# Kernel optimization log

Hardware: AMD Instinct MI355X
Metric: run time of the kernel (lower is better)

Reference implementation:

```python
import jax, jax.numpy as jnp
import numpy as np

N_GENES = 20000   # num_all_genes
D = 256           # embedding_dim
NNZ = 640000      # nonzeros in GO adjacency (~32 avg degree)
N_COND = 2000     # number of conditions
B = 16384         # batch size
MAXG = 5          # max_genes_per_condition
L = 2             # num_gnn_layers


def setup_inputs() -> dict:
    key = jax.random.key(0)
    ks = jax.random.split(key, 12)
    cond_idx = jax.random.randint(ks[0], (B,), 0, N_COND, dtype=jnp.int32)
    pert_embedding = jax.random.normal(ks[1], (N_GENES, D), jnp.float32) * 0.05
    gnn_kernels = jax.random.normal(ks[2], (L, D, D), jnp.float32) * 0.05
    mlp_w1 = jax.random.normal(ks[3], (D, D), jnp.float32) * 0.05
    mlp_b1 = jnp.zeros((D,), jnp.float32)
    mlp_w2 = jax.random.normal(ks[4], (D, D), jnp.float32) * 0.05
    mlp_b2 = jnp.zeros((D,), jnp.float32)
    adj_row = jax.random.randint(ks[5], (NNZ,), 0, N_GENES, dtype=jnp.int64)
    adj_col = jax.random.randint(ks[6], (NNZ,), 0, N_GENES, dtype=jnp.int64)
    adj_vals = jax.random.uniform(ks[7], (NNZ,), jnp.float32)
    cond_gene_idx = jax.random.randint(ks[8], (N_COND, MAXG), 0, N_GENES, dtype=jnp.int32)
    counts = jax.random.randint(ks[9], (N_COND,), 0, MAXG + 1)
    cond_gene_mask = (jnp.arange(MAXG)[None, :] < counts[:, None]).astype(jnp.float32)
    # padded slots get -1 index like the original (later clamped to 0)
    cond_gene_idx = jnp.where(cond_gene_mask > 0, cond_gene_idx, -1)
    return {
        'cond_idx': cond_idx,
        'pert_embedding': pert_embedding,
        'gnn_kernels': gnn_kernels,
        'mlp_w1': mlp_w1, 'mlp_b1': mlp_b1,
        'mlp_w2': mlp_w2, 'mlp_b2': mlp_b2,
        'adj_row': adj_row, 'adj_col': adj_col, 'adj_vals': adj_vals,
        'cond_gene_idx': cond_gene_idx, 'cond_gene_mask': cond_gene_mask,
    }


def reference(cond_idx, pert_embedding, gnn_kernels, mlp_w1, mlp_b1,
              mlp_w2, mlp_b2, adj_row, adj_col, adj_vals,
              cond_gene_idx, cond_gene_mask):
    # --- GNN over the full gene graph (sparse adjacency @ dense emb, then dense kernel) ---
    emb = pert_embedding  # [N, D]
    for i in range(L):
        # SpMM: aggregated[r] = sum_{nnz with row r} vals * emb[col]
        msgs = adj_vals[:, None] * emb[adj_col]            # [NNZ, D]
        agg = jax.ops.segment_sum(msgs, adj_row, num_segments=N_GENES)  # [N, D]
        emb = agg @ gnn_kernels[i]                          # [N, D]
        if i < L - 1:
            emb = jax.nn.relu(emb)

    # --- per-condition gather of up to MAXG gene embeddings, masked sum ---
    gidx = cond_gene_idx[cond_idx]          # [B, MAXG] int
    gmask = cond_gene_mask[cond_idx]        # [B, MAXG]
    gidx_safe = jnp.maximum(gidx, 0)
    gene_embs = emb[gidx_safe]              # [B, MAXG, D]
    summed = jnp.sum(gene_embs * gmask[:, :, None], axis=1)  # [B, D]
    n_genes = jnp.sum(gmask, axis=1)        # [B]

    # --- small MLP (applied when n_genes > 1), identity when ==1, zeros when ==0 ---
    h = jax.nn.relu(summed @ mlp_w1 + mlp_b1)
    mlp_out = jax.nn.relu(h @ mlp_w2 + mlp_b2)  # [B, D]

    n = n_genes[:, None]
    out = jnp.where(n == 0.0, 0.0, jnp.where(n == 1.0, summed, mlp_out))
    return out
```

## Files before the change

### kernel.cpp

```cpp
#include <hip/hip_runtime.h>

static constexpr int N_GENES = 20000;
static constexpr int D       = 256;
static constexpr int NNZ     = 640000;
static constexpr int BATCH   = 16384;
static constexpr int MAXG    = 5;
static constexpr int SCAN_B  = (N_GENES + 255) / 256;

using bf16x8 = __attribute__((ext_vector_type(8))) short;
using f32x4  = __attribute__((ext_vector_type(4))) float;

__device__ __forceinline__ unsigned short f2bf(float f) {
  unsigned int u = __builtin_bit_cast(unsigned int, f);
  u += 0x7fffu + ((u >> 16) & 1u);
  return (unsigned short)(u >> 16);
}
__device__ __forceinline__ float bf2f(unsigned short h) {
  unsigned int u = ((unsigned int)h) << 16;
  return __builtin_bit_cast(float, u);
}
__device__ __forceinline__ void gload16(const void* g, void* l) {
  __builtin_amdgcn_global_load_lds(
      (const __attribute__((address_space(1))) unsigned int*)g,
      (__attribute__((address_space(3))) unsigned int*)l, 16, 0, 0);
}

__global__ void zero_int(int* __restrict__ p, int n) {
  int i = blockIdx.x * blockDim.x + threadIdx.x;
  if (i < n) p[i] = 0;
}

__global__ void count_rows(const int* __restrict__ adj_row, int* __restrict__ cnt) {
  int e = blockIdx.x * blockDim.x + threadIdx.x;
  if (e < NNZ) atomicAdd(&cnt[adj_row[e]], 1);
}

__global__ __launch_bounds__(256)
void scan_partial(const int* __restrict__ cnt, int* __restrict__ bsum) {
  __shared__ int red[256];
  int b = blockIdx.x, t = threadIdx.x, i = b * 256 + t;
  red[t] = (i < N_GENES) ? cnt[i] : 0;
  __syncthreads();
  for (int off = 128; off > 0; off >>= 1) {
    if (t < off) red[t] += red[t + off];
    __syncthreads();
  }
  if (t == 0) bsum[b] = red[0];
}

__global__ __launch_bounds__(256)
void scan_final2(const int* __restrict__ cnt, const int* __restrict__ bsum,
                 int* __restrict__ row_ptr, int* __restrict__ fill_ctr) {
  __shared__ int bs[128];
  __shared__ int s[256];
  int b = blockIdx.x, t = threadIdx.x, i = b * 256 + t;
  if (t < 128) bs[t] = (t < SCAN_B) ? bsum[t] : 0;
  __syncthreads();
  for (int off = 1; off < 128; off <<= 1) {
    int v = (t >= off && t < 128) ? bs[t - off] : 0;
    __syncthreads();
    if (t < 128) bs[t] += v;
    __syncthreads();
  }
  int bpre = (b == 0) ? 0 : bs[b - 1];
  int x = (i < N_GENES) ? cnt[i] : 0;
  s[t] = x;
  __syncthreads();
  for (int off = 1; off < 256; off <<= 1) {
    int v = (t >= off) ? s[t - off] : 0;
    __syncthreads();
    s[t] += v;
    __syncthreads();
  }
  if (i < N_GENES) {
    int e = bpre + s[t] - x;
    row_ptr[i] = e;
    fill_ctr[i] = e;
  }
  if (b == 0 && t == 0) row_ptr[N_GENES] = NNZ;
}

__global__ __launch_bounds__(256)
void fused_fill_conv(const int* __restrict__ adj_row, const int* __restrict__ adj_col,
                     const float* __restrict__ vals, int* __restrict__ fill_ctr,
                     unsigned int* __restrict__ edges,
                     const float* __restrict__ gk, const float* __restrict__ w1,
                     const float* __restrict__ w2,
                     char* __restrict__ whi, char* __restrict__ wlo,
                     const float* __restrict__ pert, ushort4* __restrict__ pert_bf) {
  int b = blockIdx.x, t = threadIdx.x;
  if (b < 2500) {
    int e = b * 256 + t;
    int r = adj_row[e];
    int p = atomicAdd(&fill_ctr[r], 1);
    edges[p] = (unsigned int)adj_col[e] | ((unsigned int)f2bf(vals[e]) << 16);
  } else if (b < 2628) {
    int g = (b - 2500) * 256 + t;
    int wid = g >> 13, rest = g & 8191;
    const float* W = (wid == 0) ? gk : (wid == 1) ? gk + 65536 : (wid == 2) ? w1 : w2;
    int c  = rest >> 9;
    int nc = c >> 2, kt = c & 3;
    int o  = (rest & 511) << 4;
    int n  = o >> 7;
    int wb = (o & 127) ^ ((n & 7) << 4);
    int k  = wb >> 1;
    size_t obase = ((size_t)wid << 17) + ((size_t)c << 13) + o;
    unsigned short* ph = (unsigned short*)(whi + obase);
    unsigned short* pl = (unsigned short*)(wlo + obase);
    #pragma unroll
    for (int e2 = 0; e2 < 8; ++e2) {
      float f = W[(size_t)(kt * 64 + k + e2) * 256 + nc * 64 + n];
      unsigned short h = f2bf(f);
      ph[e2] = h;
      pl[e2] = f2bf(f - bf2f(h));
    }
  } else {
    int i = (b - 2628) * 256 + t;
    float4 v = reinterpret_cast<const float4*>(pert)[i];
    ushort4 r4;
    r4.x = f2bf(v.x); r4.y = f2bf(v.y); r4.z = f2bf(v.z); r4.w = f2bf(v.w);
    pert_bf[i] = r4;
  }
}

__global__ __launch_bounds__(256)
void spmm_csr_img(const int* __restrict__ row_ptr, const unsigned int* __restrict__ edges,
                  const unsigned short* __restrict__ src,
                  char* __restrict__ hi_img, char* __restrict__ lo_img) {
  int row = blockIdx.x * 4 + (threadIdx.x >> 6);
  int lane = threadIdx.x & 63;
  int beg = row_ptr[row], end = row_ptr[row + 1];
  const unsigned short* sp = src + lane * 4;
  float4 acc = {0.f, 0.f, 0.f, 0.f};
  int j = beg;
  for (; j + 8 <= end; j += 8) {
    unsigned int e0 = edges[j],     e1 = edges[j + 1], e2 = edges[j + 2], e3 = edges[j + 3];
    unsigned int e4 = edges[j + 4], e5 = edges[j + 5], e6 = edges[j + 6], e7 = edges[j + 7];
    ushort4 g0 = *reinterpret_cast<const ushort4*>(sp + (size_t)(e0 & 0xFFFFu) * D);
    ushort4 g1 = *reinterpret_cast<const ushort4*>(sp + (size_t)(e1 & 0xFFFFu) * D);
    ushort4 g2 = *reinterpret_cast<const ushort4*>(sp + (size_t)(e2 & 0xFFFFu) * D);
    ushort4 g3 = *reinterpret_cast<const ushort4*>(sp + (size_t)(e3 & 0xFFFFu) * D);
    ushort4 g4 = *reinterpret_cast<const ushort4*>(sp + (size_t)(e4 & 0xFFFFu) * D);
    ushort4 g5 = *reinterpret_cast<const ushort4*>(sp + (size_t)(e5 & 0xFFFFu) * D);
    ushort4 g6 = *reinterpret_cast<const ushort4*>(sp + (size_t)(e6 & 0xFFFFu) * D);
    ushort4 g7 = *reinterpret_cast<const ushort4*>(sp + (size_t)(e7 & 0xFFFFu) * D);
    float v0 = bf2f(e0 >> 16), v1 = bf2f(e1 >> 16), v2 = bf2f(e2 >> 16), v3 = bf2f(e3 >> 16);
    float v4 = bf2f(e4 >> 16), v5 = bf2f(e5 >> 16), v6 = bf2f(e6 >> 16), v7 = bf2f(e7 >> 16);
    acc.x += v0 * bf2f(g0.x); acc.y += v0 * bf2f(g0.y); acc.z += v0 * bf2f(g0.z); acc.w += v0 * bf2f(g0.w);
    acc.x += v1 * bf2f(g1.x); acc.y += v1 * bf2f(g1.y); acc.z += v1 * bf2f(g1.z); acc.w += v1 * bf2f(g1.w);
    acc.x += v2 * bf2f(g2.x); acc.y += v2 * bf2f(g2.y); acc.z += v2 * bf2f(g2.z); acc.w += v2 * bf2f(g2.w);
    acc.x += v3 * bf2f(g3.x); acc.y += v3 * bf2f(g3.y); acc.z += v3 * bf2f(g3.z); acc.w += v3 * bf2f(g3.w);
    acc.x += v4 * bf2f(g4.x); acc.y += v4 * bf2f(g4.y); acc.z += v4 * bf2f(g4.z); acc.w += v4 * bf2f(g4.w);
    acc.x += v5 * bf2f(g5.x); acc.y += v5 * bf2f(g5.y); acc.z += v5 * bf2f(g5.z); acc.w += v5 * bf2f(g5.w);
    acc.x += v6 * bf2f(g6.x); acc.y += v6 * bf2f(g6.y); acc.z += v6 * bf2f(g6.z); acc.w += v6 * bf2f(g6.w);
    acc.x += v7 * bf2f(g7.x); acc.y += v7 * bf2f(g7.y); acc.z += v7 * bf2f(g7.z); acc.w += v7 * bf2f(g7.w);
  }
  for (; j < end; ++j) {
    unsigned int e = edges[j];
    ushort4 g = *reinterpret_cast<const ushort4*>(sp + (size_t)(e & 0xFFFFu) * D);
    float v = bf2f(e >> 16);
    acc.x += v * bf2f(g.x); acc.y += v * bf2f(g.y); acc.z += v * bf2f(g.z); acc.w += v * bf2f(g.w);
  }
  int mt = row >> 7, r = row & 127, kt = lane >> 4;
  int wb = ((lane & 15) << 3) ^ ((r & 7) << 4);
  size_t off = ((size_t)(mt * 4 + kt) << 14) + (size_t)r * 128 + wb;
  float a4[4] = {acc.x, acc.y, acc.z, acc.w};
  ushort4 hi, lo;
  unsigned short* ph = (unsigned short*)&hi;
  unsigned short* pl = (unsigned short*)&lo;
  #pragma unroll
  for (int e = 0; e < 4; ++e) {
    unsigned short h = f2bf(a4[e]);
    ph[e] = h;
    pl[e] = f2bf(a4[e] - bf2f(h));
  }
  *reinterpret_cast<ushort4*>(hi_img + off) = hi;
  *reinterpret_cast<ushort4*>(lo_img + off) = lo;
}

__global__ __launch_bounds__(256)
void gather_conditions(const int* __restrict__ cond_idx, const int* __restrict__ cg_idx,
                       const float* __restrict__ cg_mask, const float* __restrict__ emb,
                       float* __restrict__ out, char* __restrict__ hi_img,
                       char* __restrict__ lo_img, float* __restrict__ ngenes) {
  int b = blockIdx.x * 4 + (threadIdx.x >> 6);
  int lane = threadIdx.x & 63;
  int c = cond_idx[b];
  float4 acc = {0.f, 0.f, 0.f, 0.f};
  float n = 0.f;
  #pragma unroll
  for (int g = 0; g < MAXG; ++g) {
    float m = cg_mask[c * MAXG + g];
    n += m;
    if (m > 0.f) {
      int gi = cg_idx[c * MAXG + g];
      float4 e = *reinterpret_cast<const float4*>(emb + (size_t)gi * D + lane * 4);
      acc.x += m * e.x; acc.y += m * e.y; acc.z += m * e.z; acc.w += m * e.w;
    }
  }
  *reinterpret_cast<float4*>(out + (size_t)b * D + lane * 4) = acc;
  int mt = b >> 7, r = b & 127, kt = lane >> 4;
  int wb = ((lane & 15) << 3) ^ ((r & 7) << 4);
  size_t off = ((size_t)(mt * 4 + kt) << 14) + (size_t)r * 128 + wb;
  float a4[4] = {acc.x, acc.y, acc.z, acc.w};
  ushort4 hi, lo;
  unsigned short* ph = (unsigned short*)&hi;
  unsigned short* pl = (unsigned short*)&lo;
  #pragma unroll
  for (int e = 0; e < 4; ++e) {
    unsigned short h = f2bf(a4[e]);
    ph[e] = h;
    pl[e] = f2bf(a4[e] - bf2f(h));
  }
  *reinterpret_cast<ushort4*>(hi_img + off) = hi;
  *reinterpret_cast<ushort4*>(lo_img + off) = lo;
  if (lane == 0) ngenes[b] = n;
}

enum Epi { E_F32, E_RELU_BF16, E_HIMG, E_SELECT };

template <Epi EP>
__global__ __launch_bounds__(256)
void gemm_bf16x3(const char* __restrict__ Ahi, const char* __restrict__ Alo,
                 const char* __restrict__ Bhi, const char* __restrict__ Blo,
                 const float* __restrict__ bias, float* __restrict__ C,
                 unsigned short* __restrict__ Cbf,
                 char* __restrict__ Ohi, char* __restrict__ Olo,
                 const float* __restrict__ ngenes, int M) {
  __shared__ __align__(16) char smem[65536];
  char* sAh = smem;
  char* sAl = smem + 16384;
  char* sBh = smem + 32768;
  char* sBl = smem + 49152;

  const int t = threadIdx.x;
  const int w = t >> 6, l = t & 63;
  const int wr = w >> 1, wc = w & 1;

  const int nwg  = gridDim.x;
  const int orig = blockIdx.x;
  const int xcd = orig & 7, boff = orig >> 3;
  const int q = nwg >> 3, r8 = nwg & 7;
  const int wgid = (xcd < r8 ? xcd * (q + 1) : r8 * (q + 1) + (xcd - r8) * q) + boff;
  const int mt = wgid >> 1, nt2 = wgid & 1;

  f32x4 acc[4][4] = {};

  const int rA = l & 15;
  const int kB = (l >> 4) << 4;
  const int xA = (rA & 7) << 4;

  for (int kt = 0; kt < 4; ++kt) {
    const char* gAh  = Ahi + ((size_t)(mt * 4 + kt) << 14);
    const char* gAl  = Alo + ((size_t)(mt * 4 + kt) << 14);
    const char* gBh0 = Bhi + ((size_t)((nt2 * 2 + 0) * 4 + kt) << 13);
    const char* gBl0 = Blo + ((size_t)((nt2 * 2 + 0) * 4 + kt) << 13);
    const char* gBh1 = Bhi + ((size_t)((nt2 * 2 + 1) * 4 + kt) << 13);
    const char* gBl1 = Blo + ((size_t)((nt2 * 2 + 1) * 4 + kt) << 13);
    #pragma unroll
    for (int j = 0; j < 4; ++j) {
      gload16(gAh + (j * 256 + t) * 16, sAh + j * 4096 + w * 1024);
      gload16(gAl + (j * 256 + t) * 16, sAl + j * 4096 + w * 1024);
    }
    #pragma unroll
    for (int j = 0; j < 2; ++j) {
      gload16(gBh0 + (j * 256 + t) * 16, sBh + j * 4096 + w * 1024);
      gload16(gBl0 + (j * 256 + t) * 16, sBl + j * 4096 + w * 1024);
    }
    #pragma unroll
    for (int j = 0; j < 2; ++j) {
      gload16(gBh1 + (j * 256 + t) * 16, sBh + 8192 + j * 4096 + w * 1024);
      gload16(gBl1 + (j * 256 + t) * 16, sBl + 8192 + j * 4096 + w * 1024);
    }
    asm volatile("s_waitcnt vmcnt(0)" ::: "memory");
    __syncthreads();
    #pragma unroll
    for (int ks = 0; ks < 2; ++ks) {
      bf16x8 ah[4], al[4], bh[4], bl[4];
      #pragma unroll
      for (int i = 0; i < 4; ++i) {
        int r   = wr * 64 + i * 16 + rA;
        int off = r * 128 + ((ks * 64 + kB) ^ xA);
        ah[i] = *(const bf16x8*)(sAh + off);
        al[i] = *(const bf16x8*)(sAl + off);
      }
      #pragma unroll
      for (int j = 0; j < 4; ++j) {
        int n   = wc * 64 + j * 16 + rA;
        int off = n * 128 + ((ks * 64 + kB) ^ xA);
        bh[j] = *(const bf16x8*)(sBh + off);
        bl[j] = *(const bf16x8*)(sBl + off);
      }
      #pragma unroll
      for (int i = 0; i < 4; ++i)
        #pragma unroll
        for (int j = 0; j < 4; ++j) {
          acc[i][j] = __builtin_amdgcn_mfma_f32_16x16x32_bf16(ah[i], bh[j], acc[i][j], 0, 0, 0);
          acc[i][j] = __builtin_amdgcn_mfma_f32_16x16x32_bf16(ah[i], bl[j], acc[i][j], 0, 0, 0);
          acc[i][j] = __builtin_amdgcn_mfma_f32_16x16x32_bf16(al[i], bh[j], acc[i][j], 0, 0, 0);
        }
    }
    __syncthreads();
  }

  const int cr = (l >> 4) << 2;
  const int cc = l & 15;
  #pragma unroll
  for (int i = 0; i < 4; ++i) {
    #pragma unroll
    for (int rr = 0; rr < 4; ++rr) {
      int rin  = wr * 64 + i * 16 + cr + rr;
      int grow = mt * 128 + rin;
      if (grow >= M) continue;
      bool wr_row = true;
      if (EP == E_SELECT) wr_row = (ngenes[grow] >= 1.5f);
      #pragma unroll
      for (int j = 0; j < 4; ++j) {
        float v    = acc[i][j][rr];
        int colin  = wc * 64 + j * 16 + cc;
        int gcol   = nt2 * 128 + colin;
        if (EP == E_HIMG || EP == E_SELECT) v += bias[gcol];
        if (EP != E_F32) v = fmaxf(v, 0.f);
        if (EP == E_HIMG) {
          int kt2 = nt2 * 2 + (colin >> 6);
          int k2  = colin & 63;
          int wb  = (k2 << 1) ^ ((rin & 7) << 4);
          size_t off = ((size_t)(mt * 4 + kt2) << 14) + (size_t)rin * 128 + wb;
          unsigned short h16 = f2bf(v);
          *(unsigned short*)(Ohi + off) = h16;
          *(unsigned short*)(Olo + off) = f2bf(v - bf2f(h16));
        } else if (EP == E_RELU_BF16) {
          Cbf[(size_t)grow * 256 + gcol] = f2bf(v);
        } else if (wr_row) {
          C[(size_t)grow * 256 + gcol] = v;
        }
      }
    }
  }
}

extern "C" void kernel_launch(void* const* d_in, const int* in_sizes, int n_in,
                              void* d_out, int out_size, void* d_ws, size_t ws_size,
                              hipStream_t stream) {
  const int*   cond_idx = (const int*)d_in[0];
  const float* pert     = (const float*)d_in[1];
  const float* gnn_k    = (const float*)d_in[2];
  const float* w1       = (const float*)d_in[3];
  const float* b1       = (const float*)d_in[4];
  const float* w2       = (const float*)d_in[5];
  const float* b2       = (const float*)d_in[6];
  const int*   adj_row  = (const int*)d_in[7];
  const int*   adj_col  = (const int*)d_in[8];
  const float* adj_vals = (const float*)d_in[9];
  const int*   cg_idx   = (const int*)d_in[10];
  const float* cg_mask  = (const float*)d_in[11];
  float* out = (float*)d_out;

  char* w = (char*)d_ws;
  auto alloc = [&](size_t bytes) {
    void* p = w;
    w += (bytes + 255) & ~size_t(255);
    return p;
  };
  constexpr int MT_G = (N_GENES + 127) / 128;
  constexpr int MT_B = BATCH / 128;
  char*         aggHi   = (char*)alloc((size_t)MT_G * 4 * 16384);
  char*         aggLo   = (char*)alloc((size_t)MT_G * 4 * 16384);
  float*        embf    = (float*)alloc((size_t)N_GENES * D * 4);
  char*         sumHi   = (char*)alloc((size_t)MT_B * 4 * 16384);
  char*         sumLo   = (char*)alloc((size_t)MT_B * 4 * 16384);
  char*         hHi     = (char*)alloc((size_t)MT_B * 4 * 16384);
  char*         hLo     = (char*)alloc((size_t)MT_B * 4 * 16384);
  char*         wHi     = (char*)alloc((size_t)4 << 17);
  char*         wLo     = (char*)alloc((size_t)4 << 17);
  unsigned int* edges   = (unsigned int*)alloc((size_t)NNZ * 4);
  int*          cnt     = (int*)alloc((size_t)N_GENES * 4);
  int*          row_ptr = (int*)alloc((size_t)(N_GENES + 4) * 4);
  int*          fill_ctr= (int*)alloc((size_t)N_GENES * 4);
  int*          bsum    = (int*)alloc((size_t)128 * 4);
  float*        ngenes  = (float*)alloc((size_t)BATCH * 4);

  unsigned short* pert_bf = (unsigned short*)hHi;
  unsigned short* embf_bf = (unsigned short*)embf;

  zero_int<<<(N_GENES + 255) / 256, 256, 0, stream>>>(cnt, N_GENES);
  count_rows<<<NNZ / 256, 256, 0, stream>>>(adj_row, cnt);
  scan_partial<<<SCAN_B, 256, 0, stream>>>(cnt, bsum);
  scan_final2<<<SCAN_B, 256, 0, stream>>>(cnt, bsum, row_ptr, fill_ctr);
  fused_fill_conv<<<2500 + 128 + 5000, 256, 0, stream>>>(
      adj_row, adj_col, adj_vals, fill_ctr, edges,
      gnn_k, w1, w2, wHi, wLo, pert, (ushort4*)pert_bf);

  spmm_csr_img<<<N_GENES / 4, 256, 0, stream>>>(row_ptr, edges, pert_bf, aggHi, aggLo);
  gemm_bf16x3<E_RELU_BF16><<<2 * MT_G, 256, 0, stream>>>(
      aggHi, aggLo, wHi, wLo, nullptr, nullptr, embf_bf, nullptr, nullptr, nullptr, N_GENES);

  spmm_csr_img<<<N_GENES / 4, 256, 0, stream>>>(row_ptr, edges, embf_bf, aggHi, aggLo);
  gemm_bf16x3<E_F32><<<2 * MT_G, 256, 0, stream>>>(
      aggHi, aggLo, wHi + (1 << 17), wLo + (1 << 17), nullptr, embf, nullptr, nullptr, nullptr, nullptr, N_GENES);

  gather_conditions<<<BATCH / 4, 256, 0, stream>>>(cond_idx, cg_idx, cg_mask, embf,
                                                   out, sumHi, sumLo, ngenes);

  gemm_bf16x3<E_HIMG><<<2 * MT_B, 256, 0, stream>>>(
      sumHi, sumLo, wHi + (2 << 17), wLo + (2 << 17), b1, nullptr, nullptr, hHi, hLo, nullptr, BATCH);

  gemm_bf16x3<E_SELECT><<<2 * MT_B, 256, 0, stream>>>(
      hHi, hLo, wHi + (3 << 17), wLo + (3 << 17), b2, out, nullptr, nullptr, nullptr, ngenes, BATCH);
}
```

Before: 314.6 us.

## Fuse condition gather into first MLP GEMM and merge scan kernels

Moves the per-condition masked gather of gene embeddings into the first MLP GEMM. Each block builds its bf16 hi/lo A tile directly in shared memory, which removes the separate gather kernel and its sum-image round trip through global memory. The two-pass prefix scan becomes a single kernel in which each block recomputes its own prefix from the counts. Zeroing the counts now uses hipMemsetAsync. The cost is that both column-half blocks redo the same gather, and that gather now runs serially before the MFMA work in each k-step.

After: 326.2 us. 3.7% more time.

```diff
diff --git a/kernel.cpp b/kernel.cpp
--- a/kernel.cpp
+++ b/kernel.cpp
@@ -8,6 +8,7 @@
 static constexpr int SCAN_B  = (N_GENES + 255) / 256;
 
 using bf16x8 = __attribute__((ext_vector_type(8))) short;
+using us8    = __attribute__((ext_vector_type(8))) unsigned short;
 using f32x4  = __attribute__((ext_vector_type(4))) float;
 
 __device__ __forceinline__ unsigned short f2bf(float f) {
@@ -25,44 +26,26 @@
       (__attribute__((address_space(3))) unsigned int*)l, 16, 0, 0);
 }
 
-__global__ void zero_int(int* __restrict__ p, int n) {
-  int i = blockIdx.x * blockDim.x + threadIdx.x;
-  if (i < n) p[i] = 0;
-}
-
 __global__ void count_rows(const int* __restrict__ adj_row, int* __restrict__ cnt) {
   int e = blockIdx.x * blockDim.x + threadIdx.x;
   if (e < NNZ) atomicAdd(&cnt[adj_row[e]], 1);
 }
 
 __global__ __launch_bounds__(256)
-void scan_partial(const int* __restrict__ cnt, int* __restrict__ bsum) {
-  __shared__ int red[256];
+void scan_one(const int* __restrict__ cnt, int* __restrict__ row_ptr,
+              int* __restrict__ fill_ctr) {
+  __shared__ int s[256];
   int b = blockIdx.x, t = threadIdx.x, i = b * 256 + t;
-  red[t] = (i < N_GENES) ? cnt[i] : 0;
+  int pre_t = 0;
+  for (int c = 0; c < b; ++c) pre_t += cnt[c * 256 + t];
+  s[t] = pre_t;
   __syncthreads();
   for (int off = 128; off > 0; off >>= 1) {
-    if (t < off) red[t] += red[t + off];
-    __syncthreads();
-  }
-  if (t == 0) bsum[b] = red[0];
-}
-
-__global__ __launch_bounds__(256)
-void scan_final2(const int* __restrict__ cnt, const int* __restrict__ bsum,
-                 int* __restrict__ row_ptr, int* __restrict__ fill_ctr) {
-  __shared__ int bs[128];
-  __shared__ int s[256];
-  int b = blockIdx.x, t = threadIdx.x, i = b * 256 + t;
-  if (t < 128) bs[t] = (t < SCAN_B) ? bsum[t] : 0;
+    if (t < off) s[t] += s[t + off];
+    __syncthreads();
+  }
+  int bpre = s[0];
   __syncthreads();
-  for (int off = 1; off < 128; off <<= 1) {
-    int v = (t >= off && t < 128) ? bs[t - off] : 0;
-    __syncthreads();
-    if (t < 128) bs[t] += v;
-    __syncthreads();
-  }
-  int bpre = (b == 0) ? 0 : bs[b - 1];
   int x = (i < N_GENES) ? cnt[i] : 0;
   s[t] = x;
   __syncthreads();
@@ -178,46 +161,13 @@
   *reinterpret_cast<ushort4*>(lo_img + off) = lo;
 }
 
-__global__ __launch_bounds__(256)
-void gather_conditions(const int* __restrict__ cond_idx, const int* __restrict__ cg_idx,
-                       const float* __restrict__ cg_mask, const float* __restrict__ emb,
-                       float* __restrict__ out, char* __restrict__ hi_img,
-                       char* __restrict__ lo_img, float* __restrict__ ngenes) {
-  int b = blockIdx.x * 4 + (threadIdx.x >> 6);
-  int lane = threadIdx.x & 63;
-  int c = cond_idx[b];
-  float4 acc = {0.f, 0.f, 0.f, 0.f};
-  float n = 0.f;
-  #pragma unroll
-  for (int g = 0; g < MAXG; ++g) {
-    float m = cg_mask[c * MAXG + g];
-    n += m;
-    if (m > 0.f) {
-      int gi = cg_idx[c * MAXG + g];
-      float4 e = *reinterpret_cast<const float4*>(emb + (size_t)gi * D + lane * 4);
-      acc.x += m * e.x; acc.y += m * e.y; acc.z += m * e.z; acc.w += m * e.w;
-    }
-  }
-  *reinterpret_cast<float4*>(out + (size_t)b * D + lane * 4) = acc;
-  int mt = b >> 7, r = b & 127, kt = lane >> 4;
-  int wb = ((lane & 15) << 3) ^ ((r & 7) << 4);
-  size_t off = ((size_t)(mt * 4 + kt) << 14) + (size_t)r * 128 + wb;
-  float a4[4] = {acc.x, acc.y, acc.z, acc.w};
-  ushort4 hi, lo;
-  unsigned short* ph = (unsigned short*)&hi;
-  unsigned short* pl = (unsigned short*)&lo;
-  #pragma unroll
-  for (int e = 0; e < 4; ++e) {
-    unsigned short h = f2bf(a4[e]);
-    ph[e] = h;
-    pl[e] = f2bf(a4[e] - bf2f(h));
-  }
-  *reinterpret_cast<ushort4*>(hi_img + off) = hi;
-  *reinterpret_cast<ushort4*>(lo_img + off) = lo;
-  if (lane == 0) ngenes[b] = n;
-}
-
-enum Epi { E_F32, E_RELU_BF16, E_HIMG, E_SELECT };
+__device__ __forceinline__ int xcd_swizzle(int orig, int nwg) {
+  int xcd = orig & 7, boff = orig >> 3;
+  int q = nwg >> 3, r8 = nwg & 7;
+  return (xcd < r8 ? xcd * (q + 1) : r8 * (q + 1) + (xcd - r8) * q) + boff;
+}
+
+enum Epi { E_F32, E_RELU_BF16, E_SELECT };
 
 template <Epi EP>
 __global__ __launch_bounds__(256)
@@ -225,7 +175,6 @@
                  const char* __restrict__ Bhi, const char* __restrict__ Blo,
                  const float* __restrict__ bias, float* __restrict__ C,
                  unsigned short* __restrict__ Cbf,
-                 char* __restrict__ Ohi, char* __restrict__ Olo,
                  const float* __restrict__ ngenes, int M) {
   __shared__ __align__(16) char smem[65536];
   char* sAh = smem;
@@ -236,16 +185,10 @@
   const int t = threadIdx.x;
   const int w = t >> 6, l = t & 63;
   const int wr = w >> 1, wc = w & 1;
-
-  const int nwg  = gridDim.x;
-  const int orig = blockIdx.x;
-  const int xcd = orig & 7, boff = orig >> 3;
-  const int q = nwg >> 3, r8 = nwg & 7;
-  const int wgid = (xcd < r8 ? xcd * (q + 1) : r8 * (q + 1) + (xcd - r8) * q) + boff;
+  const int wgid = xcd_swizzle(blockIdx.x, gridDim.x);
   const int mt = wgid >> 1, nt2 = wgid & 1;
 
   f32x4 acc[4][4] = {};
-
   const int rA = l & 15;
   const int kB = (l >> 4) << 4;
   const int xA = (rA & 7) << 4;
@@ -266,9 +209,6 @@
     for (int j = 0; j < 2; ++j) {
       gload16(gBh0 + (j * 256 + t) * 16, sBh + j * 4096 + w * 1024);
       gload16(gBl0 + (j * 256 + t) * 16, sBl + j * 4096 + w * 1024);
-    }
-    #pragma unroll
-    for (int j = 0; j < 2; ++j) {
       gload16(gBh1 + (j * 256 + t) * 16, sBh + 8192 + j * 4096 + w * 1024);
       gload16(gBl1 + (j * 256 + t) * 16, sBl + 8192 + j * 4096 + w * 1024);
     }
@@ -279,15 +219,13 @@
       bf16x8 ah[4], al[4], bh[4], bl[4];
       #pragma unroll
       for (int i = 0; i < 4; ++i) {
-        int r   = wr * 64 + i * 16 + rA;
-        int off = r * 128 + ((ks * 64 + kB) ^ xA);
+        int off = (wr * 64 + i * 16 + rA) * 128 + ((ks * 64 + kB) ^ xA);
         ah[i] = *(const bf16x8*)(sAh + off);
         al[i] = *(const bf16x8*)(sAl + off);
       }
       #pragma unroll
       for (int j = 0; j < 4; ++j) {
-        int n   = wc * 64 + j * 16 + rA;
-        int off = n * 128 + ((ks * 64 + kB) ^ xA);
+        int off = (wc * 64 + j * 16 + rA) * 128 + ((ks * 64 + kB) ^ xA);
         bh[j] = *(const bf16x8*)(sBh + off);
         bl[j] = *(const bf16x8*)(sBl + off);
       }
@@ -316,24 +254,148 @@
       if (EP == E_SELECT) wr_row = (ngenes[grow] >= 1.5f);
       #pragma unroll
       for (int j = 0; j < 4; ++j) {
-        float v    = acc[i][j][rr];
-        int colin  = wc * 64 + j * 16 + cc;
-        int gcol   = nt2 * 128 + colin;
-        if (EP == E_HIMG || EP == E_SELECT) v += bias[gcol];
+        float v   = acc[i][j][rr];
+        int gcol  = nt2 * 128 + wc * 64 + j * 16 + cc;
+        if (EP == E_SELECT) v += bias[gcol];
         if (EP != E_F32) v = fmaxf(v, 0.f);
-        if (EP == E_HIMG) {
-          int kt2 = nt2 * 2 + (colin >> 6);
-          int k2  = colin & 63;
-          int wb  = (k2 << 1) ^ ((rin & 7) << 4);
-          size_t off = ((size_t)(mt * 4 + kt2) << 14) + (size_t)rin * 128 + wb;
-          unsigned short h16 = f2bf(v);
-          *(unsigned short*)(Ohi + off) = h16;
-          *(unsigned short*)(Olo + off) = f2bf(v - bf2f(h16));
-        } else if (EP == E_RELU_BF16) {
+        if (EP == E_RELU_BF16) {
           Cbf[(size_t)grow * 256 + gcol] = f2bf(v);
         } else if (wr_row) {
           C[(size_t)grow * 256 + gcol] = v;
         }
+      }
+    }
+  }
+}
+
+__global__ __launch_bounds__(256)
+void gemm_mlp1(const int* __restrict__ cond_idx, const int* __restrict__ cg_idx,
+               const float* __restrict__ cg_mask, const float* __restrict__ embf,
+               const char* __restrict__ Bhi, const char* __restrict__ Blo,
+               const float* __restrict__ bias, float* __restrict__ out,
+               float* __restrict__ ngenes,
+               char* __restrict__ Ohi, char* __restrict__ Olo) {
+  __shared__ __align__(16) char smem[65536];
+  char* sAh = smem;
+  char* sAl = smem + 16384;
+  char* sBh = smem + 32768;
+  char* sBl = smem + 49152;
+
+  const int t = threadIdx.x;
+  const int w = t >> 6, l = t & 63;
+  const int wr = w >> 1, wc = w & 1;
+  const int wgid = xcd_swizzle(blockIdx.x, gridDim.x);
+  const int mt = wgid >> 1, nt2 = wgid & 1;
+
+  const int gr = t >> 1, ghalf = t & 1;
+  const int grow = mt * 128 + gr;
+  const int gc = cond_idx[grow];
+
+  f32x4 acc[4][4] = {};
+  const int rA = l & 15;
+  const int kB = (l >> 4) << 4;
+  const int xA = (rA & 7) << 4;
+
+  for (int kt = 0; kt < 4; ++kt) {
+    const char* gBh0 = Bhi + ((size_t)((nt2 * 2 + 0) * 4 + kt) << 13);
+    const char* gBl0 = Blo + ((size_t)((nt2 * 2 + 0) * 4 + kt) << 13);
+    const char* gBh1 = Bhi + ((size_t)((nt2 * 2 + 1) * 4 + kt) << 13);
+    const char* gBl1 = Blo + ((size_t)((nt2 * 2 + 1) * 4 + kt) << 13);
+    #pragma unroll
+    for (int j = 0; j < 2; ++j) {
+      gload16(gBh0 + (j * 256 + t) * 16, sBh + j * 4096 + w * 1024);
+      gload16(gBl0 + (j * 256 + t) * 16, sBl + j * 4096 + w * 1024);
+      gload16(gBh1 + (j * 256 + t) * 16, sBh + 8192 + j * 4096 + w * 1024);
+      gload16(gBl1 + (j * 256 + t) * 16, sBl + 8192 + j * 4096 + w * 1024);
+    }
+    float4 a[8] = {};
+    float n = 0.f;
+    #pragma unroll
+    for (int g = 0; g < MAXG; ++g) {
+      float m = cg_mask[gc * MAXG + g];
+      n += m;
+      if (m > 0.f) {
+        const float4* e = reinterpret_cast<const float4*>(
+            embf + (size_t)cg_idx[gc * MAXG + g] * 256 + kt * 64 + ghalf * 32);
+        #pragma unroll
+        for (int q = 0; q < 8; ++q) {
+          float4 ev = e[q];
+          a[q].x += m * ev.x; a[q].y += m * ev.y;
+          a[q].z += m * ev.z; a[q].w += m * ev.w;
+        }
+      }
+    }
+    if (nt2 == 0) {
+      float4* o = reinterpret_cast<float4*>(out + (size_t)grow * 256 + kt * 64 + ghalf * 32);
+      #pragma unroll
+      for (int q = 0; q < 8; ++q) o[q] = a[q];
+      if (kt == 0 && ghalf == 0) ngenes[grow] = n;
+    }
+    const int xr = (gr & 7) << 4;
+    const float* av = reinterpret_cast<const float*>(a);
+    #pragma unroll
+    for (int q = 0; q < 4; ++q) {
+      us8 hv, lv;
+      #pragma unroll
+      for (int jj = 0; jj < 8; ++jj) {
+        float vv = av[q * 8 + jj];
+        unsigned short h = f2bf(vv);
+        hv[jj] = h;
+        lv[jj] = f2bf(vv - bf2f(h));
+      }
+      int byteoff = gr * 128 + (((ghalf * 32 + q * 8) << 1) ^ xr);
+      *reinterpret_cast<us8*>(sAh + byteoff) = hv;
+      *reinterpret_cast<us8*>(sAl + byteoff) = lv;
+    }
+    asm volatile("s_waitcnt vmcnt(0)" ::: "memory");
+    __syncthreads();
+    #pragma unroll
+    for (int ks = 0; ks < 2; ++ks) {
+      bf16x8 ah[4], al[4], bh[4], bl[4];
+      #pragma unroll
+      for (int i = 0; i < 4; ++i) {
+        int off = (wr * 64 + i * 16 + rA) * 128 + ((ks * 64 + kB) ^ xA);
+        ah[i] = *(const bf16x8*)(sAh + off);
+        al[i] = *(const bf16x8*)(sAl + off);
+      }
+      #pragma unroll
+      for (int j = 0; j < 4; ++j) {
+        int off = (wc * 64 + j * 16 + rA) * 128 + ((ks * 64 + kB) ^ xA);
+        bh[j] = *(const bf16x8*)(sBh + off);
+        bl[j] = *(const bf16x8*)(sBl + off);
+      }
+      #pragma unroll
+      for (int i = 0; i < 4; ++i)
+        #pragma unroll
+        for (int j = 0; j < 4; ++j) {
+          acc[i][j] = __builtin_amdgcn_mfma_f32_16x16x32_bf16(ah[i], bh[j], acc[i][j], 0, 0, 0);
+          acc[i][j] = __builtin_amdgcn_mfma_f32_16x16x32_bf16(ah[i], bl[j], acc[i][j], 0, 0, 0);
+          acc[i][j] = __builtin_amdgcn_mfma_f32_16x16x32_bf16(al[i], bh[j], acc[i][j], 0, 0, 0);
+        }
+    }
+    __syncthreads();
+  }
+
+  const int cr = (l >> 4) << 2;
+  const int cc = l & 15;
+  #pragma unroll
+  for (int i = 0; i < 4; ++i) {
+    #pragma unroll
+    for (int rr = 0; rr < 4; ++rr) {
+      int rin = wr * 64 + i * 16 + cr + rr;
+      #pragma unroll
+      for (int j = 0; j < 4; ++j) {
+        float v   = acc[i][j][rr];
+        int colin = wc * 64 + j * 16 + cc;
+        int gcol  = nt2 * 128 + colin;
+        v = fmaxf(v + bias[gcol], 0.f);
+        int kt2 = nt2 * 2 + (colin >> 6);
+        int k2  = colin & 63;
+        int wb  = (k2 << 1) ^ ((rin & 7) << 4);
+        size_t off = ((size_t)(mt * 4 + kt2) << 14) + (size_t)rin * 128 + wb;
+        unsigned short h16 = f2bf(v);
+        *(unsigned short*)(Ohi + off) = h16;
+        *(unsigned short*)(Olo + off) = f2bf(v - bf2f(h16));
       }
     }
   }
@@ -367,8 +429,6 @@
   char*         aggHi   = (char*)alloc((size_t)MT_G * 4 * 16384);
   char*         aggLo   = (char*)alloc((size_t)MT_G * 4 * 16384);
   float*        embf    = (float*)alloc((size_t)N_GENES * D * 4);
-  char*         sumHi   = (char*)alloc((size_t)MT_B * 4 * 16384);
-  char*         sumLo   = (char*)alloc((size_t)MT_B * 4 * 16384);
   char*         hHi     = (char*)alloc((size_t)MT_B * 4 * 16384);
   char*         hLo     = (char*)alloc((size_t)MT_B * 4 * 16384);
   char*         wHi     = (char*)alloc((size_t)4 << 17);
@@ -377,34 +437,31 @@
   int*          cnt     = (int*)alloc((size_t)N_GENES * 4);
   int*          row_ptr = (int*)alloc((size_t)(N_GENES + 4) * 4);
   int*          fill_ctr= (int*)alloc((size_t)N_GENES * 4);
-  int*          bsum    = (int*)alloc((size_t)128 * 4);
   float*        ngenes  = (float*)alloc((size_t)BATCH * 4);
-
-  unsigned short* pert_bf = (unsigned short*)hHi;
+  char*         pertbf_buf = (char*)alloc((size_t)N_GENES * D * 2);
+
+  unsigned short* pert_bf = (unsigned short*)pertbf_buf;
   unsigned short* embf_bf = (unsigned short*)embf;
 
-  zero_int<<<(N_GENES + 255) / 256, 256, 0, stream>>>(cnt, N_GENES);
+  hipMemsetAsync(cnt, 0, (size_t)N_GENES * 4, stream);
   count_rows<<<NNZ / 256, 256, 0, stream>>>(adj_row, cnt);
-  scan_partial<<<SCAN_B, 256, 0, stream>>>(cnt, bsum);
-  scan_final2<<<SCAN_B, 256, 0, stream>>>(cnt, bsum, row_ptr, fill_ctr);
+  scan_one<<<SCAN_B, 256, 0, stream>>>(cnt, row_ptr, fill_ctr);
   fused_fill_conv<<<2500 + 128 + 5000, 256, 0, stream>>>(
       adj_row, adj_col, adj_vals, fill_ctr, edges,
       gnn_k, w1, w2, wHi, wLo, pert, (ushort4*)pert_bf);
 
   spmm_csr_img<<<N_GENES / 4, 256, 0, stream>>>(row_ptr, edges, pert_bf, aggHi, aggLo);
   gemm_bf16x3<E_RELU_BF16><<<2 * MT_G, 256, 0, stream>>>(
-      aggHi, aggLo, wHi, wLo, nullptr, nullptr, embf_bf, nullptr, nullptr, nullptr, N_GENES);
+      aggHi, aggLo, wHi, wLo, nullptr, nullptr, embf_bf, nullptr, N_GENES);
 
   spmm_csr_img<<<N_GENES / 4, 256, 0, stream>>>(row_ptr, edges, embf_bf, aggHi, aggLo);
   gemm_bf16x3<E_F32><<<2 * MT_G, 256, 0, stream>>>(
-      aggHi, aggLo, wHi + (1 << 17), wLo + (1 << 17), nullptr, embf, nullptr, nullptr, nullptr, nullptr, N_GENES);
-
-  gather_conditions<<<BATCH / 4, 256, 0, stream>>>(cond_idx, cg_idx, cg_mask, embf,
-                                                   out, sumHi, sumLo, ngenes);
-
-  gemm_bf16x3<E_HIMG><<<2 * MT_B, 256, 0, stream>>>(
-      sumHi, sumLo, wHi + (2 << 17), wLo + (2 << 17), b1, nullptr, nullptr, hHi, hLo, nullptr, BATCH);
+      aggHi, aggLo, wHi + (1 << 17), wLo + (1 << 17), nullptr, embf, nullptr, nullptr, N_GENES);
+
+  gemm_mlp1<<<2 * MT_B, 256, 0, stream>>>(
+      cond_idx, cg_idx, cg_mask, embf, wHi + (2 << 17), wLo + (2 << 17),
+      b1, out, ngenes, hHi, hLo);
 
   gemm_bf16x3<E_SELECT><<<2 * MT_B, 256, 0, stream>>>(
-      hHi, hLo, wHi + (3 << 17), wLo + (3 << 17), b2, out, nullptr, nullptr, nullptr, ngenes, BATCH);
-}
+      hHi, hLo, wHi + (3 << 17), wLo + (3 << 17), b2, out, nullptr, ngenes, BATCH);
+}
```

## Sort CSR edges within each row by column range for gather locality

Applied to the files above, without the earlier changes.

Edges are now bucketed by row and by one of 8 column ranges, so each row's neighbours are grouped by source-row region. This gives the SpMM gathers better cache locality. The scan grows eightfold and gets a middle single-block pass, and the counter zeroing moves to hipMemsetAsync. The GEMM swizzle is tidied into a helper, and the pert_bf scratch buffer moves from hHi to sumHi. The cost is a larger prefix-sum and one extra kernel launch.

After: 313.2 us. About the same (-0.4%).

```diff
diff --git a/kernel.cpp b/kernel.cpp
--- a/kernel.cpp
+++ b/kernel.cpp
@@ -5,7 +5,9 @@
 static constexpr int NNZ     = 640000;
 static constexpr int BATCH   = 16384;
 static constexpr int MAXG    = 5;
-static constexpr int SCAN_B  = (N_GENES + 255) / 256;
+static constexpr int NR      = 8;
+static constexpr int NB      = N_GENES * NR;
+static constexpr int SCAN_BLKS = NB / 256;
 
 using bf16x8 = __attribute__((ext_vector_type(8))) short;
 using f32x4  = __attribute__((ext_vector_type(4))) float;
@@ -24,22 +26,22 @@
       (const __attribute__((address_space(1))) unsigned int*)g,
       (__attribute__((address_space(3))) unsigned int*)l, 16, 0, 0);
 }
-
-__global__ void zero_int(int* __restrict__ p, int n) {
-  int i = blockIdx.x * blockDim.x + threadIdx.x;
-  if (i < n) p[i] = 0;
-}
-
-__global__ void count_rows(const int* __restrict__ adj_row, int* __restrict__ cnt) {
-  int e = blockIdx.x * blockDim.x + threadIdx.x;
-  if (e < NNZ) atomicAdd(&cnt[adj_row[e]], 1);
+__device__ __forceinline__ unsigned colrange(int col) {
+  return ((unsigned)col * 26215u) >> 26;
+}
+
+__global__ void count_buckets(const int* __restrict__ adj_row,
+                              const int* __restrict__ adj_col, int* __restrict__ cnt) {
+  int e = blockIdx.x * 256 + threadIdx.x;
+  int r = adj_row[e];
+  atomicAdd(&cnt[(r << 3) | colrange(adj_col[e])], 1);
 }
 
 __global__ __launch_bounds__(256)
 void scan_partial(const int* __restrict__ cnt, int* __restrict__ bsum) {
   __shared__ int red[256];
-  int b = blockIdx.x, t = threadIdx.x, i = b * 256 + t;
-  red[t] = (i < N_GENES) ? cnt[i] : 0;
+  int b = blockIdx.x, t = threadIdx.x;
+  red[t] = cnt[b * 256 + t];
   __syncthreads();
   for (int off = 128; off > 0; off >>= 1) {
     if (t < off) red[t] += red[t + off];
@@ -48,22 +50,28 @@
   if (t == 0) bsum[b] = red[0];
 }
 
-__global__ __launch_bounds__(256)
-void scan_final2(const int* __restrict__ cnt, const int* __restrict__ bsum,
-                 int* __restrict__ row_ptr, int* __restrict__ fill_ctr) {
-  __shared__ int bs[128];
+__global__ __launch_bounds__(1024)
+void scan_mid(const int* __restrict__ bsum, int* __restrict__ bpre) {
+  __shared__ int s[1024];
+  int t = threadIdx.x;
+  int x = (t < SCAN_BLKS) ? bsum[t] : 0;
+  s[t] = x;
+  __syncthreads();
+  for (int off = 1; off < 1024; off <<= 1) {
+    int v = (t >= off) ? s[t - off] : 0;
+    __syncthreads();
+    s[t] += v;
+    __syncthreads();
+  }
+  if (t < SCAN_BLKS) bpre[t] = s[t] - x;
+}
+
+__global__ __launch_bounds__(256)
+void scan_final(const int* __restrict__ cnt, const int* __restrict__ bpre,
+                int* __restrict__ bptr, int* __restrict__ fill_ctr) {
   __shared__ int s[256];
   int b = blockIdx.x, t = threadIdx.x, i = b * 256 + t;
-  if (t < 128) bs[t] = (t < SCAN_B) ? bsum[t] : 0;
-  __syncthreads();
-  for (int off = 1; off < 128; off <<= 1) {
-    int v = (t >= off && t < 128) ? bs[t - off] : 0;
-    __syncthreads();
-    if (t < 128) bs[t] += v;
-    __syncthreads();
-  }
-  int bpre = (b == 0) ? 0 : bs[b - 1];
-  int x = (i < N_GENES) ? cnt[i] : 0;
+  int x = cnt[i];
   s[t] = x;
   __syncthreads();
   for (int off = 1; off < 256; off <<= 1) {
@@ -72,12 +80,10 @@
     s[t] += v;
     __syncthreads();
   }
-  if (i < N_GENES) {
-    int e = bpre + s[t] - x;
-    row_ptr[i] = e;
-    fill_ctr[i] = e;
-  }
-  if (b == 0 && t == 0) row_ptr[N_GENES] = NNZ;
+  int e = bpre[b] + s[t] - x;
+  bptr[i] = e;
+  fill_ctr[i] = e;
+  if (b == 0 && t == 0) bptr[NB] = NNZ;
 }
 
 __global__ __launch_bounds__(256)
@@ -92,8 +98,9 @@
   if (b < 2500) {
     int e = b * 256 + t;
     int r = adj_row[e];
-    int p = atomicAdd(&fill_ctr[r], 1);
-    edges[p] = (unsigned int)adj_col[e] | ((unsigned int)f2bf(vals[e]) << 16);
+    int col = adj_col[e];
+    int p = atomicAdd(&fill_ctr[(r << 3) | colrange(col)], 1);
+    edges[p] = (unsigned int)col | ((unsigned int)f2bf(vals[e]) << 16);
   } else if (b < 2628) {
     int g = (b - 2500) * 256 + t;
     int wid = g >> 13, rest = g & 8191;
@@ -124,12 +131,12 @@
 }
 
 __global__ __launch_bounds__(256)
-void spmm_csr_img(const int* __restrict__ row_ptr, const unsigned int* __restrict__ edges,
+void spmm_csr_img(const int* __restrict__ bptr, const unsigned int* __restrict__ edges,
                   const unsigned short* __restrict__ src,
                   char* __restrict__ hi_img, char* __restrict__ lo_img) {
   int row = blockIdx.x * 4 + (threadIdx.x >> 6);
   int lane = threadIdx.x & 63;
-  int beg = row_ptr[row], end = row_ptr[row + 1];
+  int beg = bptr[row << 3], end = bptr[(row << 3) + 8];
   const unsigned short* sp = src + lane * 4;
   float4 acc = {0.f, 0.f, 0.f, 0.f};
   int j = beg;
@@ -217,6 +224,12 @@
   if (lane == 0) ngenes[b] = n;
 }
 
+__device__ __forceinline__ int xcd_swizzle(int orig, int nwg) {
+  int xcd = orig & 7, boff = orig >> 3;
+  int q = nwg >> 3, r8 = nwg & 7;
+  return (xcd < r8 ? xcd * (q + 1) : r8 * (q + 1) + (xcd - r8) * q) + boff;
+}
+
 enum Epi { E_F32, E_RELU_BF16, E_HIMG, E_SELECT };
 
 template <Epi EP>
@@ -236,16 +249,10 @@
   const int t = threadIdx.x;
   const int w = t >> 6, l = t & 63;
   const int wr = w >> 1, wc = w & 1;
-
-  const int nwg  = gridDim.x;
-  const int orig = blockIdx.x;
-  const int xcd = orig & 7, boff = orig >> 3;
-  const int q = nwg >> 3, r8 = nwg & 7;
-  const int wgid = (xcd < r8 ? xcd * (q + 1) : r8 * (q + 1) + (xcd - r8) * q) + boff;
+  const int wgid = xcd_swizzle(blockIdx.x, gridDim.x);
   const int mt = wgid >> 1, nt2 = wgid & 1;
 
   f32x4 acc[4][4] = {};
-
   const int rA = l & 15;
   const int kB = (l >> 4) << 4;
   const int xA = (rA & 7) << 4;
@@ -266,9 +273,6 @@
     for (int j = 0; j < 2; ++j) {
       gload16(gBh0 + (j * 256 + t) * 16, sBh + j * 4096 + w * 1024);
       gload16(gBl0 + (j * 256 + t) * 16, sBl + j * 4096 + w * 1024);
-    }
-    #pragma unroll
-    for (int j = 0; j < 2; ++j) {
       gload16(gBh1 + (j * 256 + t) * 16, sBh + 8192 + j * 4096 + w * 1024);
       gload16(gBl1 + (j * 256 + t) * 16, sBl + 8192 + j * 4096 + w * 1024);
     }
@@ -279,15 +283,13 @@
       bf16x8 ah[4], al[4], bh[4], bl[4];
       #pragma unroll
       for (int i = 0; i < 4; ++i) {
-        int r   = wr * 64 + i * 16 + rA;
-        int off = r * 128 + ((ks * 64 + kB) ^ xA);
+        int off = (wr * 64 + i * 16 + rA) * 128 + ((ks * 64 + kB) ^ xA);
         ah[i] = *(const bf16x8*)(sAh + off);
         al[i] = *(const bf16x8*)(sAl + off);
       }
       #pragma unroll
       for (int j = 0; j < 4; ++j) {
-        int n   = wc * 64 + j * 16 + rA;
-        int off = n * 128 + ((ks * 64 + kB) ^ xA);
+        int off = (wc * 64 + j * 16 + rA) * 128 + ((ks * 64 + kB) ^ xA);
         bh[j] = *(const bf16x8*)(sBh + off);
         bl[j] = *(const bf16x8*)(sBl + off);
       }
@@ -316,9 +318,9 @@
       if (EP == E_SELECT) wr_row = (ngenes[grow] >= 1.5f);
       #pragma unroll
       for (int j = 0; j < 4; ++j) {
-        float v    = acc[i][j][rr];
-        int colin  = wc * 64 + j * 16 + cc;
-        int gcol   = nt2 * 128 + colin;
+        float v   = acc[i][j][rr];
+        int colin = wc * 64 + j * 16 + cc;
+        int gcol  = nt2 * 128 + colin;
         if (EP == E_HIMG || EP == E_SELECT) v += bias[gcol];
         if (EP != E_F32) v = fmaxf(v, 0.f);
         if (EP == E_HIMG) {
@@ -374,28 +376,30 @@
   char*         wHi     = (char*)alloc((size_t)4 << 17);
   char*         wLo     = (char*)alloc((size_t)4 << 17);
   unsigned int* edges   = (unsigned int*)alloc((size_t)NNZ * 4);
-  int*          cnt     = (int*)alloc((size_t)N_GENES * 4);
-  int*          row_ptr = (int*)alloc((size_t)(N_GENES + 4) * 4);
-  int*          fill_ctr= (int*)alloc((size_t)N_GENES * 4);
-  int*          bsum    = (int*)alloc((size_t)128 * 4);
+  int*          cnt     = (int*)alloc((size_t)NB * 4);
+  int*          bptr    = (int*)alloc((size_t)(NB + 4) * 4);
+  int*          fill_ctr= (int*)alloc((size_t)NB * 4);
+  int*          bsum    = (int*)alloc((size_t)1024 * 4);
+  int*          bpre    = (int*)alloc((size_t)1024 * 4);
   float*        ngenes  = (float*)alloc((size_t)BATCH * 4);
 
-  unsigned short* pert_bf = (unsigned short*)hHi;
+  unsigned short* pert_bf = (unsigned short*)sumHi;
   unsigned short* embf_bf = (unsigned short*)embf;
 
-  zero_int<<<(N_GENES + 255) / 256, 256, 0, stream>>>(cnt, N_GENES);
-  count_rows<<<NNZ / 256, 256, 0, stream>>>(adj_row, cnt);
-  scan_partial<<<SCAN_B, 256, 0, stream>>>(cnt, bsum);
-  scan_final2<<<SCAN_B, 256, 0, stream>>>(cnt, bsum, row_ptr, fill_ctr);
+  hipMemsetAsync(cnt, 0, (size_t)NB * 4, stream);
+  count_buckets<<<NNZ / 256, 256, 0, stream>>>(adj_row, adj_col, cnt);
+  scan_partial<<<SCAN_BLKS, 256, 0, stream>>>(cnt, bsum);
+  scan_mid<<<1, 1024, 0, stream>>>(bsum, bpre);
+  scan_final<<<SCAN_BLKS, 256, 0, stream>>>(cnt, bpre, bptr, fill_ctr);
   fused_fill_conv<<<2500 + 128 + 5000, 256, 0, stream>>>(
       adj_row, adj_col, adj_vals, fill_ctr, edges,
       gnn_k, w1, w2, wHi, wLo, pert, (ushort4*)pert_bf);
 
-  spmm_csr_img<<<N_GENES / 4, 256, 0, stream>>>(row_ptr, edges, pert_bf, aggHi, aggLo);
+  spmm_csr_img<<<N_GENES / 4, 256, 0, stream>>>(bptr, edges, pert_bf, aggHi, aggLo);
   gemm_bf16x3<E_RELU_BF16><<<2 * MT_G, 256, 0, stream>>>(
       aggHi, aggLo, wHi, wLo, nullptr, nullptr, embf_bf, nullptr, nullptr, nullptr, N_GENES);
 
-  spmm_csr_img<<<N_GENES / 4, 256, 0, stream>>>(row_ptr, edges, embf_bf, aggHi, aggLo);
+  spmm_csr_img<<<N_GENES / 4, 256, 0, stream>>>(bptr, edges, embf_bf, aggHi, aggLo);
   gemm_bf16x3<E_F32><<<2 * MT_G, 256, 0, stream>>>(
       aggHi, aggLo, wHi + (1 << 17), wLo + (1 << 17), nullptr, embf, nullptr, nullptr, nullptr, nullptr, N_GENES);
 
```
